# Optimization experiments

Hardware: AMD Instinct MI355X
Metric: run time of the kernel (lower is better)

The kernel has to match this reference:

```python
import jax, jax.numpy as jnp
import numpy as np


def _quat_raw_mul(a, b):
    aw, ax, ay, az = a[..., 0], a[..., 1], a[..., 2], a[..., 3]
    bw, bx, by, bz = b[..., 0], b[..., 1], b[..., 2], b[..., 3]
    ow = aw * bw - ax * bx - ay * by - az * bz
    ox = aw * bx + ax * bw + ay * bz - az * by
    oy = aw * by - ax * bz + ay * bw + az * bx
    oz = aw * bz + ax * by - ay * bx + az * bw
    return jnp.stack([ow, ox, oy, oz], axis=-1)


def _standardize(q):
    # pytorch3d.quaternion_multiply standardizes sign so w >= 0
    return jnp.where(q[..., :1] < 0, -q, q)


def _quat_apply(q, v):
    # rotate points v by unit quaternions q: q * (0, v) * conj(q), take imaginary part
    pv = jnp.concatenate([jnp.zeros_like(v[..., :1]), v], axis=-1)
    conj = q * jnp.asarray([1.0, -1.0, -1.0, -1.0], dtype=q.dtype)
    return _quat_raw_mul(_quat_raw_mul(q, pv), conj)[..., 1:]


def _axis_angle_to_quat(aa):
    # pytorch3d.axis_angle_to_quaternion with small-angle Taylor branch
    angle = jnp.linalg.norm(aa, axis=-1, keepdims=True)
    half = 0.5 * angle
    eps = 1e-6
    small = jnp.abs(angle) < eps
    safe_angle = jnp.where(small, jnp.ones_like(angle), angle)
    k = jnp.where(small, 0.5 - angle * angle / 48.0, jnp.sin(half) / safe_angle)
    return jnp.concatenate([jnp.cos(half), aa * k], axis=-1)


def _matrix_to_quat(M):
    # pytorch3d.matrix_to_quaternion (candidate-selection form), vectorized
    m00, m11, m22 = M[..., 0, 0], M[..., 1, 1], M[..., 2, 2]
    q_abs = jnp.sqrt(jax.nn.relu(jnp.stack([
        1.0 + m00 + m11 + m22,
        1.0 + m00 - m11 - m22,
        1.0 - m00 + m11 - m22,
        1.0 - m00 - m11 + m22], axis=-1)))
    c0 = jnp.stack([q_abs[..., 0] ** 2, M[..., 2, 1] - M[..., 1, 2], M[..., 0, 2] - M[..., 2, 0], M[..., 1, 0] - M[..., 0, 1]], axis=-1)
    c1 = jnp.stack([M[..., 2, 1] - M[..., 1, 2], q_abs[..., 1] ** 2, M[..., 1, 0] + M[..., 0, 1], M[..., 0, 2] + M[..., 2, 0]], axis=-1)
    c2 = jnp.stack([M[..., 0, 2] - M[..., 2, 0], M[..., 1, 0] + M[..., 0, 1], q_abs[..., 2] ** 2, M[..., 2, 1] + M[..., 1, 2]], axis=-1)
    c3 = jnp.stack([M[..., 1, 0] - M[..., 0, 1], M[..., 2, 0] + M[..., 0, 2], M[..., 2, 1] + M[..., 1, 2], q_abs[..., 3] ** 2], axis=-1)
    cands = jnp.stack([c0, c1, c2, c3], axis=-2)  # (..., 4 candidates, 4)
    flr = 0.1
    cands = cands / (2.0 * jnp.maximum(q_abs[..., None], flr))
    idx = jnp.argmax(q_abs, axis=-1)
    return jnp.take_along_axis(cands, idx[..., None, None], axis=-2)[..., 0, :]


def _or6d_to_quat(d6):
    a1, a2 = d6[..., :3], d6[..., 3:]
    b1 = a1 / jnp.linalg.norm(a1, axis=-1, keepdims=True)
    a2p = a2 - jnp.sum(b1 * a2, axis=-1, keepdims=True) * b1
    b2 = a2p / jnp.linalg.norm(a2p, axis=-1, keepdims=True)
    b3 = jnp.cross(b1, b2)
    M = jnp.stack([b1, b2, b3], axis=-2)  # (..., 3, 3)
    return _matrix_to_quat(M)


def setup_inputs() -> dict:
    key = jax.random.key(0)
    k1, k2, k3, k4 = jax.random.split(key, 4)
    N, T, J = 256, 1024, 24
    return {
        'root_rvel': jax.random.normal(k1, (N, T, 1, 1), dtype=jnp.float32),
        'local_pos': jax.random.normal(k2, (N, T + 1, J, 3), dtype=jnp.float32),
        'local_rot': jax.random.normal(k3, (N, T + 1, J, 6), dtype=jnp.float32),
        'root_vel': jax.random.normal(k4, (N, T, 1, 2), dtype=jnp.float32),
    }


def reference(root_rvel, local_pos, local_rot, root_vel):
    # cumulative root yaw angle with zero initial frame: (N, T+1, 1, 1)
    r = jnp.cumsum(root_rvel, axis=1)
    r = jnp.concatenate([jnp.zeros_like(r[:, :1]), r], axis=1)
    # axis-angle about Y axis -> quaternion (N, T+1, 1, 4)
    aa = r * jnp.asarray([0.0, 1.0, 0.0], dtype=r.dtype)
    rotation = _axis_angle_to_quat(aa)
    # local 6D rotations -> quaternions (N, T+1, J, 4)
    local_q = _or6d_to_quat(local_rot)
    global_rot = _standardize(_quat_raw_mul(rotation, local_q))
    relative_pos = _quat_apply(rotation, local_pos)
    # lift XZ hip velocity to 3D, rotate into world frame, integrate
    zeros_y = jnp.zeros_like(root_vel[..., :1])
    v3 = jnp.concatenate([root_vel[..., :1], zeros_y, root_vel[..., 1:]], axis=-1)  # (N,T,1,3)
    v3w = _quat_apply(rotation[:, :-1], v3)
    pos_xz = jnp.concatenate([jnp.zeros_like(v3w[:, :1]), jnp.cumsum(v3w, axis=1)], axis=1)  # (N,T+1,1,3)
    global_pos = relative_pos + pos_xz
    return global_pos, global_rot
```

## Files before the change

kernel.cpp:

```cpp
#include <hip/hip_runtime.h>

#define N_SEQ 256
#define T_LEN 1024
#define TP1   (T_LEN + 1)
#define J_NUM 24
#define ITEMS (TP1 * J_NUM)
#define TOTAL_ITEMS (N_SEQ * ITEMS)
#define TOTAL_GROUPS (TOTAL_ITEMS / 4)
#define GP_TOTAL (N_SEQ * TP1 * J_NUM * 3)

__device__ __forceinline__ float block_scan_incl(float v, float* wsum, int tid) {
    const int lane = tid & 63;
    const int wid  = tid >> 6;
    #pragma unroll
    for (int off = 1; off < 64; off <<= 1) {
        float u = __shfl_up(v, off, 64);
        if (lane >= off) v += u;
    }
    if (lane == 63) wsum[wid] = v;
    __syncthreads();
    if (tid == 0) {
        float acc = 0.0f;
        #pragma unroll
        for (int i = 0; i < 16; ++i) { float t = wsum[i]; wsum[i] = acc; acc += t; }
    }
    __syncthreads();
    return v + wsum[wid];
}

extern "C" __global__ void __launch_bounds__(1024)
scan_kernel(const float* __restrict__ root_rvel,
            const float* __restrict__ root_vel,
            float2* __restrict__ ws_quat,
            float2* __restrict__ ws_pos)
{
    const int n   = blockIdx.x;
    const int tid = threadIdx.x;

    __shared__ float  r_s[TP1];
    __shared__ float2 quat_s[TP1];
    __shared__ float  ws_a[16], ws_b[16], ws_c[16];

    {
        float v = root_rvel[n * T_LEN + tid];
        float incl = block_scan_incl(v, ws_a, tid);
        if (tid == 0) r_s[0] = 0.0f;
        r_s[tid + 1] = incl;
    }
    __syncthreads();

    for (int idx = tid; idx < TP1; idx += 1024) {
        float r     = r_s[idx];
        float angle = fabsf(r);
        float half  = 0.5f * angle;
        float k = (angle < 1e-6f) ? (0.5f - angle * angle * (1.0f / 48.0f))
                                  : (__builtin_sinf(half) / angle);
        float2 q = make_float2(__builtin_cosf(half), r * k);
        quat_s[idx] = q;
        ws_quat[n * TP1 + idx] = q;
    }
    __syncthreads();

    {
        float2 vel = ((const float2*)root_vel)[n * T_LEN + tid];
        float2 q   = quat_s[tid];
        float  w = q.x, y = q.y;
        float t1x = w * vel.x + y * vel.y;
        float t1z = w * vel.y - y * vel.x;
        float ax  = t1x * w + t1z * y;
        float az  = t1z * w - t1x * y;
        float ix = block_scan_incl(ax, ws_b, tid);
        float iz = block_scan_incl(az, ws_c, tid);
        if (tid == 0) ws_pos[n * TP1] = make_float2(0.0f, 0.0f);
        ws_pos[n * TP1 + tid + 1] = make_float2(ix, iz);
    }
}

extern "C" __global__ void __launch_bounds__(256)
elem_kernel(const float4* __restrict__ rot4,
            const float4* __restrict__ pos4,
            const float2* __restrict__ ws_quat,
            const float2* __restrict__ ws_pos,
            float4* __restrict__ out_rot4,
            float4* __restrict__ out_pos4)
{
    const unsigned g = blockIdx.x * 256u + threadIdx.x;
    if (g >= TOTAL_GROUPS) return;
    const unsigned base = g * 4u;
    const unsigned seq  = base / ITEMS;
    const unsigned t    = (base - seq * ITEMS) / J_NUM;

    const float2 qt = ws_quat[seq * TP1 + t];
    const float2 ps = ws_pos [seq * TP1 + t];
    const float w = qt.x, yq = qt.y;
    const float wwyy = w * w + yq * yq;

    float rf[24], pf[12], opf[12];
    {
        const float4* rp = rot4 + (size_t)g * 6;
        #pragma unroll
        for (int i = 0; i < 6; ++i) {
            float4 a = rp[i];
            rf[4*i+0] = a.x; rf[4*i+1] = a.y; rf[4*i+2] = a.z; rf[4*i+3] = a.w;
        }
        const float4* pp = pos4 + (size_t)g * 3;
        #pragma unroll
        for (int i = 0; i < 3; ++i) {
            float4 a = pp[i];
            pf[4*i+0] = a.x; pf[4*i+1] = a.y; pf[4*i+2] = a.z; pf[4*i+3] = a.w;
        }
    }

    float4* orp = out_rot4 + (size_t)g * 4;

    #pragma unroll
    for (int k = 0; k < 4; ++k) {
        float a1x = rf[6*k+0], a1y = rf[6*k+1], a1z = rf[6*k+2];
        float a2x = rf[6*k+3], a2y = rf[6*k+4], a2z = rf[6*k+5];

        float inv1 = 1.0f / sqrtf(a1x * a1x + a1y * a1y + a1z * a1z);
        float b1x = a1x * inv1, b1y = a1y * inv1, b1z = a1z * inv1;
        float dp  = b1x * a2x + b1y * a2y + b1z * a2z;
        float px  = a2x - dp * b1x, py = a2y - dp * b1y, pz = a2z - dp * b1z;
        float inv2 = 1.0f / sqrtf(px * px + py * py + pz * pz);
        float b2x = px * inv2, b2y = py * inv2, b2z = pz * inv2;
        float b3x = b1y * b2z - b1z * b2y;
        float b3y = b1z * b2x - b1x * b2z;
        float b3z = b1x * b2y - b1y * b2x;

        float m00 = b1x, m01 = b1y, m02 = b1z;
        float m10 = b2x, m11 = b2y, m12 = b2z;
        float m20 = b3x, m21 = b3y, m22 = b3z;

        float qa0 = sqrtf(fmaxf(1.0f + m00 + m11 + m22, 0.0f));
        float qa1 = sqrtf(fmaxf(1.0f + m00 - m11 - m22, 0.0f));
        float qa2 = sqrtf(fmaxf(1.0f - m00 + m11 - m22, 0.0f));
        float qa3 = sqrtf(fmaxf(1.0f - m00 - m11 + m22, 0.0f));

        int best = 0; float bv = qa0;
        if (qa1 > bv) { best = 1; bv = qa1; }
        if (qa2 > bv) { best = 2; bv = qa2; }
        if (qa3 > bv) { best = 3; bv = qa3; }

        float lw, lx, ly, lz;
        if (best == 0)      { lw = qa0 * qa0;  lx = m21 - m12;  ly = m02 - m20;  lz = m10 - m01; }
        else if (best == 1) { lw = m21 - m12;  lx = qa1 * qa1;  ly = m10 + m01;  lz = m02 + m20; }
        else if (best == 2) { lw = m02 - m20;  lx = m10 + m01;  ly = qa2 * qa2;  lz = m21 + m12; }
        else                { lw = m10 - m01;  lx = m20 + m02;  ly = m21 + m12;  lz = qa3 * qa3; }
        float invd = 1.0f / (2.0f * fmaxf(bv, 0.1f));
        lw *= invd; lx *= invd; ly *= invd; lz *= invd;

        float ow = w * lw - yq * ly;
        float ox = w * lx + yq * lz;
        float oy = w * ly + yq * lw;
        float oz = w * lz - yq * lx;
        if (ow < 0.0f) { ow = -ow; ox = -ox; oy = -oy; oz = -oz; }
        orp[k] = make_float4(ow, ox, oy, oz);

        float vx = pf[3*k+0], vy = pf[3*k+1], vz = pf[3*k+2];
        float t1x = w * vx + yq * vz;
        float t1z = w * vz - yq * vx;
        opf[3*k+0] = t1x * w + t1z * yq + ps.x;
        opf[3*k+1] = wwyy * vy;
        opf[3*k+2] = t1z * w - t1x * yq + ps.y;
    }

    float4* opp = out_pos4 + (size_t)g * 3;
    #pragma unroll
    for (int i = 0; i < 3; ++i)
        opp[i] = make_float4(opf[4*i+0], opf[4*i+1], opf[4*i+2], opf[4*i+3]);
}

extern "C" void kernel_launch(void* const* d_in, const int* in_sizes, int n_in,
                              void* d_out, int out_size, void* d_ws, size_t ws_size,
                              hipStream_t stream) {
    (void)in_sizes; (void)n_in; (void)ws_size; (void)out_size;
    const float* root_rvel = (const float*)d_in[0];
    const float* local_pos = (const float*)d_in[1];
    const float* local_rot = (const float*)d_in[2];
    const float* root_vel  = (const float*)d_in[3];
    float* out = (float*)d_out;

    float2* ws_quat = (float2*)d_ws;
    float2* ws_pos  = ws_quat + (size_t)N_SEQ * TP1;

    scan_kernel<<<N_SEQ, 1024, 0, stream>>>(root_rvel, root_vel, ws_quat, ws_pos);

    elem_kernel<<<TOTAL_GROUPS / 256, 256, 0, stream>>>(
        (const float4*)local_rot, (const float4*)local_pos,
        ws_quat, ws_pos,
        (float4*)(out + GP_TOTAL),
        (float4*)out);
}
```

Baseline: 349.6 us.

## Stage element inputs through LDS with one item per thread and packed workspace

The element kernel now gives each thread a single joint item instead of four. Rot and pos inputs are loaded coalesced as float4 into shared memory with padded strides, and position outputs are staged through shared memory so global stores are coalesced float4 writes. The scan kernel packs the yaw quaternion and the integrated position into one float4 workspace entry, so each item needs only one lookup. Fast hardware rsq/sqrt/rcp intrinsics replace the IEEE divides and sqrts, and the sqrt is deferred to the chosen candidate, at a small precision risk and with extra barriers and LDS use.

```diff
diff --git a/kernel.cpp b/kernel.cpp
--- a/kernel.cpp
+++ b/kernel.cpp
@@ -4,10 +4,10 @@
 #define T_LEN 1024
 #define TP1   (T_LEN + 1)
 #define J_NUM 24
-#define ITEMS (TP1 * J_NUM)
-#define TOTAL_ITEMS (N_SEQ * ITEMS)
-#define TOTAL_GROUPS (TOTAL_ITEMS / 4)
+#define SEQ_ITEMS (TP1 * J_NUM)
+#define TOTAL_ITEMS (N_SEQ * SEQ_ITEMS)
 #define GP_TOTAL (N_SEQ * TP1 * J_NUM * 3)
+#define NBLOCKS (TOTAL_ITEMS / 256)
 
 __device__ __forceinline__ float block_scan_incl(float v, float* wsum, int tid) {
     const int lane = tid & 63;
@@ -31,8 +31,7 @@
 extern "C" __global__ void __launch_bounds__(1024)
 scan_kernel(const float* __restrict__ root_rvel,
             const float* __restrict__ root_vel,
-            float2* __restrict__ ws_quat,
-            float2* __restrict__ ws_pos)
+            float4* __restrict__ ws4)
 {
     const int n   = blockIdx.x;
     const int tid = threadIdx.x;
@@ -55,9 +54,7 @@
         float half  = 0.5f * angle;
         float k = (angle < 1e-6f) ? (0.5f - angle * angle * (1.0f / 48.0f))
                                   : (__builtin_sinf(half) / angle);
-        float2 q = make_float2(__builtin_cosf(half), r * k);
-        quat_s[idx] = q;
-        ws_quat[n * TP1 + idx] = q;
+        quat_s[idx] = make_float2(__builtin_cosf(half), r * k);
     }
     __syncthreads();
 
@@ -71,104 +68,121 @@
         float az  = t1z * w - t1x * y;
         float ix = block_scan_incl(ax, ws_b, tid);
         float iz = block_scan_incl(az, ws_c, tid);
-        if (tid == 0) ws_pos[n * TP1] = make_float2(0.0f, 0.0f);
-        ws_pos[n * TP1 + tid + 1] = make_float2(ix, iz);
+        float2 qn = quat_s[tid + 1];
+        ws4[n * TP1 + tid + 1] = make_float4(qn.x, qn.y, ix, iz);
+        if (tid == 0) ws4[n * TP1] = make_float4(1.0f, 0.0f, 0.0f, 0.0f);
     }
 }
 
 extern "C" __global__ void __launch_bounds__(256)
 elem_kernel(const float4* __restrict__ rot4,
             const float4* __restrict__ pos4,
-            const float2* __restrict__ ws_quat,
-            const float2* __restrict__ ws_pos,
+            const float4* __restrict__ ws4,
             float4* __restrict__ out_rot4,
             float4* __restrict__ out_pos4)
 {
-    const unsigned g = blockIdx.x * 256u + threadIdx.x;
-    if (g >= TOTAL_GROUPS) return;
-    const unsigned base = g * 4u;
-    const unsigned seq  = base / ITEMS;
-    const unsigned t    = (base - seq * ITEMS) / J_NUM;
-
-    const float2 qt = ws_quat[seq * TP1 + t];
-    const float2 ps = ws_pos [seq * TP1 + t];
-    const float w = qt.x, yq = qt.y;
-    const float wwyy = w * w + yq * yq;
-
-    float rf[24], pf[12], opf[12];
+    __shared__ float  s_rot[256 * 7];
+    __shared__ float  s_pos[256 * 5];
+    __shared__ float4 s_out4[192];
+    float* s_out = (float*)s_out4;
+
+    const int tid = threadIdx.x;
+    const unsigned blk = blockIdx.x;
+
     {
-        const float4* rp = rot4 + (size_t)g * 6;
+        const float4* rbase = rot4 + (size_t)blk * 384;
         #pragma unroll
-        for (int i = 0; i < 6; ++i) {
-            float4 a = rp[i];
-            rf[4*i+0] = a.x; rf[4*i+1] = a.y; rf[4*i+2] = a.z; rf[4*i+3] = a.w;
+        for (int it = 0; it < 2; ++it) {
+            int q = tid + it * 256;
+            if (q < 384) {
+                float4 v = rbase[q];
+                int f = 4 * q;
+                float vv[4] = {v.x, v.y, v.z, v.w};
+                #pragma unroll
+                for (int m = 0; m < 4; ++m) {
+                    int ff = f + m;
+                    s_rot[7 * (ff / 6) + (ff % 6)] = vv[m];
+                }
+            }
         }
-        const float4* pp = pos4 + (size_t)g * 3;
+    }
+    if (tid < 192) {
+        float4 v = (pos4 + (size_t)blk * 192)[tid];
+        int f = 4 * tid;
+        float vv[4] = {v.x, v.y, v.z, v.w};
         #pragma unroll
-        for (int i = 0; i < 3; ++i) {
-            float4 a = pp[i];
-            pf[4*i+0] = a.x; pf[4*i+1] = a.y; pf[4*i+2] = a.z; pf[4*i+3] = a.w;
+        for (int m = 0; m < 4; ++m) {
+            int ff = f + m;
+            s_pos[5 * (ff / 3) + (ff % 3)] = vv[m];
         }
     }
-
-    float4* orp = out_rot4 + (size_t)g * 4;
-
-    #pragma unroll
-    for (int k = 0; k < 4; ++k) {
-        float a1x = rf[6*k+0], a1y = rf[6*k+1], a1z = rf[6*k+2];
-        float a2x = rf[6*k+3], a2y = rf[6*k+4], a2z = rf[6*k+5];
-
-        float inv1 = 1.0f / sqrtf(a1x * a1x + a1y * a1y + a1z * a1z);
-        float b1x = a1x * inv1, b1y = a1y * inv1, b1z = a1z * inv1;
-        float dp  = b1x * a2x + b1y * a2y + b1z * a2z;
-        float px  = a2x - dp * b1x, py = a2y - dp * b1y, pz = a2z - dp * b1z;
-        float inv2 = 1.0f / sqrtf(px * px + py * py + pz * pz);
-        float b2x = px * inv2, b2y = py * inv2, b2z = pz * inv2;
-        float b3x = b1y * b2z - b1z * b2y;
-        float b3y = b1z * b2x - b1x * b2z;
-        float b3z = b1x * b2y - b1y * b2x;
-
-        float m00 = b1x, m01 = b1y, m02 = b1z;
-        float m10 = b2x, m11 = b2y, m12 = b2z;
-        float m20 = b3x, m21 = b3y, m22 = b3z;
-
-        float qa0 = sqrtf(fmaxf(1.0f + m00 + m11 + m22, 0.0f));
-        float qa1 = sqrtf(fmaxf(1.0f + m00 - m11 - m22, 0.0f));
-        float qa2 = sqrtf(fmaxf(1.0f - m00 + m11 - m22, 0.0f));
-        float qa3 = sqrtf(fmaxf(1.0f - m00 - m11 + m22, 0.0f));
-
-        int best = 0; float bv = qa0;
-        if (qa1 > bv) { best = 1; bv = qa1; }
-        if (qa2 > bv) { best = 2; bv = qa2; }
-        if (qa3 > bv) { best = 3; bv = qa3; }
-
-        float lw, lx, ly, lz;
-        if (best == 0)      { lw = qa0 * qa0;  lx = m21 - m12;  ly = m02 - m20;  lz = m10 - m01; }
-        else if (best == 1) { lw = m21 - m12;  lx = qa1 * qa1;  ly = m10 + m01;  lz = m02 + m20; }
-        else if (best == 2) { lw = m02 - m20;  lx = m10 + m01;  ly = qa2 * qa2;  lz = m21 + m12; }
-        else                { lw = m10 - m01;  lx = m20 + m02;  ly = m21 + m12;  lz = qa3 * qa3; }
-        float invd = 1.0f / (2.0f * fmaxf(bv, 0.1f));
-        lw *= invd; lx *= invd; ly *= invd; lz *= invd;
-
-        float ow = w * lw - yq * ly;
-        float ox = w * lx + yq * lz;
-        float oy = w * ly + yq * lw;
-        float oz = w * lz - yq * lx;
-        if (ow < 0.0f) { ow = -ow; ox = -ox; oy = -oy; oz = -oz; }
-        orp[k] = make_float4(ow, ox, oy, oz);
-
-        float vx = pf[3*k+0], vy = pf[3*k+1], vz = pf[3*k+2];
-        float t1x = w * vx + yq * vz;
-        float t1z = w * vz - yq * vx;
-        opf[3*k+0] = t1x * w + t1z * yq + ps.x;
-        opf[3*k+1] = wwyy * vy;
-        opf[3*k+2] = t1z * w - t1x * yq + ps.y;
-    }
-
-    float4* opp = out_pos4 + (size_t)g * 3;
-    #pragma unroll
-    for (int i = 0; i < 3; ++i)
-        opp[i] = make_float4(opf[4*i+0], opf[4*i+1], opf[4*i+2], opf[4*i+3]);
+    __syncthreads();
+
+    const unsigned a   = blk * 256u + (unsigned)tid;
+    const unsigned seq = a / (unsigned)SEQ_ITEMS;
+    const unsigned rem = a - seq * (unsigned)SEQ_ITEMS;
+    const unsigned t   = rem / (unsigned)J_NUM;
+
+    const float4 wq = ws4[seq * (unsigned)TP1 + t];
+    const float w = wq.x, yq = wq.y;
+
+    const int rb = 7 * tid;
+    float a1x = s_rot[rb + 0], a1y = s_rot[rb + 1], a1z = s_rot[rb + 2];
+    float a2x = s_rot[rb + 3], a2y = s_rot[rb + 4], a2z = s_rot[rb + 5];
+
+    float inv1 = __builtin_amdgcn_rsqf(a1x * a1x + a1y * a1y + a1z * a1z);
+    float b1x = a1x * inv1, b1y = a1y * inv1, b1z = a1z * inv1;
+    float dp  = b1x * a2x + b1y * a2y + b1z * a2z;
+    float px  = a2x - dp * b1x, py = a2y - dp * b1y, pz = a2z - dp * b1z;
+    float inv2 = __builtin_amdgcn_rsqf(px * px + py * py + pz * pz);
+    float b2x = px * inv2, b2y = py * inv2, b2z = pz * inv2;
+    float b3x = b1y * b2z - b1z * b2y;
+    float b3y = b1z * b2x - b1x * b2z;
+    float b3z = b1x * b2y - b1y * b2x;
+
+    float m00 = b1x, m01 = b1y, m02 = b1z;
+    float m10 = b2x, m11 = b2y, m12 = b2z;
+    float m20 = b3x, m21 = b3y, m22 = b3z;
+
+    float s0 = fmaxf(1.0f + m00 + m11 + m22, 0.0f);
+    float s1 = fmaxf(1.0f + m00 - m11 - m22, 0.0f);
+    float s2 = fmaxf(1.0f - m00 + m11 - m22, 0.0f);
+    float s3 = fmaxf(1.0f - m00 - m11 + m22, 0.0f);
+
+    int best = 0; float bs = s0;
+    if (s1 > bs) { best = 1; bs = s1; }
+    if (s2 > bs) { best = 2; bs = s2; }
+    if (s3 > bs) { best = 3; bs = s3; }
+
+    float lw, lx, ly, lz;
+    if (best == 0)      { lw = bs;         lx = m21 - m12;  ly = m02 - m20;  lz = m10 - m01; }
+    else if (best == 1) { lw = m21 - m12;  lx = bs;         ly = m10 + m01;  lz = m02 + m20; }
+    else if (best == 2) { lw = m02 - m20;  lx = m10 + m01;  ly = bs;         lz = m21 + m12; }
+    else                { lw = m10 - m01;  lx = m20 + m02;  ly = m21 + m12;  lz = bs;        }
+
+    float bv   = __builtin_amdgcn_sqrtf(bs);
+    float invd = __builtin_amdgcn_rcpf(2.0f * fmaxf(bv, 0.1f));
+    lw *= invd; lx *= invd; ly *= invd; lz *= invd;
+
+    float ow = w * lw - yq * ly;
+    float ox = w * lx + yq * lz;
+    float oy = w * ly + yq * lw;
+    float oz = w * lz - yq * lx;
+    if (ow < 0.0f) { ow = -ow; ox = -ox; oy = -oy; oz = -oz; }
+    out_rot4[a] = make_float4(ow, ox, oy, oz);
+
+    const int pb = 5 * tid;
+    float vx = s_pos[pb + 0], vy = s_pos[pb + 1], vz = s_pos[pb + 2];
+    float t1x = w * vx + yq * vz;
+    float t1z = w * vz - yq * vx;
+    s_out[3 * tid + 0] = t1x * w + t1z * yq + wq.z;
+    s_out[3 * tid + 1] = (w * w + yq * yq) * vy;
+    s_out[3 * tid + 2] = t1z * w - t1x * yq + wq.w;
+    __syncthreads();
+
+    if (tid < 192) {
+        out_pos4[(size_t)blk * 192 + tid] = s_out4[tid];
+    }
 }
 
 extern "C" void kernel_launch(void* const* d_in, const int* in_sizes, int n_in,
@@ -181,14 +195,12 @@
     const float* root_vel  = (const float*)d_in[3];
     float* out = (float*)d_out;
 
-    float2* ws_quat = (float2*)d_ws;
-    float2* ws_pos  = ws_quat + (size_t)N_SEQ * TP1;
-
-    scan_kernel<<<N_SEQ, 1024, 0, stream>>>(root_rvel, root_vel, ws_quat, ws_pos);
-
-    elem_kernel<<<TOTAL_GROUPS / 256, 256, 0, stream>>>(
-        (const float4*)local_rot, (const float4*)local_pos,
-        ws_quat, ws_pos,
+    float4* ws4 = (float4*)d_ws;
+
+    scan_kernel<<<N_SEQ, 1024, 0, stream>>>(root_rvel, root_vel, ws4);
+
+    elem_kernel<<<NBLOCKS, 256, 0, stream>>>(
+        (const float4*)local_rot, (const float4*)local_pos, ws4,
         (float4*)(out + GP_TOTAL),
         (float4*)out);
 }
```

After: 334.7 us. 4.3% less time.
